# Performance work log

Hardware: AMD Instinct MI355X
Metric: run time of the kernel (lower is better)

The kernel has to match this reference:

```python
import jax, jax.numpy as jnp
import numpy as np

NUM_CLASSES = 22
CLIP_LENGTH = 256.0
OVERLAP_THRESH = 0.5
EPS = 1.1920929e-07  # torch.finfo(float32).eps
BOUNDS_LO = jnp.array([0., 15., 30., 60., 96., 256.], dtype=jnp.float32)
BOUNDS_HI = jnp.array([30., 60., 120., 240., 768., 768.], dtype=jnp.float32)


def setup_inputs() -> dict:
    key = jax.random.key(0)
    ks = jax.random.split(key, 9)
    B, K, C, N = 8, 100000, NUM_CLASSES, 32
    loc_data = jax.random.uniform(ks[0], (B, K, 2), jnp.float32)
    conf_data = jax.random.normal(ks[1], (B, K, C), jnp.float32)
    prop_loc_data = jax.random.uniform(ks[2], (B, K, 2), jnp.float32)
    prop_conf_data = jax.random.normal(ks[3], (B, K, C), jnp.float32)
    center_data = jax.random.normal(ks[4], (B, K, 1), jnp.float32)
    # priors: [K,2] = (center in [0,1], pyramid-level index 0..5)
    centers = (jnp.arange(K, dtype=jnp.float32) + 0.5) / K
    levels = jax.random.randint(ks[5], (K,), 0, 6).astype(jnp.float32)
    priors = jnp.stack([centers, levels], axis=-1)
    # targets: [B,N,3] = (start, end, label), label in 1..C-1
    starts = jax.random.uniform(ks[6], (B, N), jnp.float32, 0.0, 0.8)
    lens = jax.random.uniform(ks[7], (B, N), jnp.float32, 0.02, 0.3)
    ends = jnp.clip(starts + lens, 0.0, 1.0)
    labels = jax.random.randint(ks[8], (B, N), 1, C).astype(jnp.float32)
    targets = jnp.stack([starts, ends, labels], axis=-1)
    return {"loc_data": loc_data, "conf_data": conf_data,
            "prop_loc_data": prop_loc_data, "prop_conf_data": prop_conf_data,
            "center_data": center_data, "priors": priors, "targets": targets}


def _calc_iou(pred, tgt):
    # pred/tgt: [..., 2] = (left, right) distances; 1-D segment IoU
    inter = jnp.minimum(pred[..., 0], tgt[..., 0]) + jnp.minimum(pred[..., 1], tgt[..., 1])
    union = pred[..., 0] + pred[..., 1] + tgt[..., 0] + tgt[..., 1] - inter
    return inter / jnp.maximum(union, EPS)


def _giou_elem(pred, tgt):
    inter = jnp.minimum(pred[..., 0], tgt[..., 0]) + jnp.minimum(pred[..., 1], tgt[..., 1])
    union = pred[..., 0] + pred[..., 1] + tgt[..., 0] + tgt[..., 1] - inter
    ious = inter / jnp.maximum(union, EPS)
    ac = jnp.maximum(pred[..., 0], tgt[..., 0]) + jnp.maximum(pred[..., 1], tgt[..., 1])
    gious = ious - (ac - union) / jnp.maximum(ac, EPS)
    return 1.0 - gious


def _focal_sum(logits, tgt):
    # FocalLoss_Ori: softmax probs, pt = p[target]+1e-10, alpha[0]=0.25, alpha[1:]=0.75,
    # loss = -alpha_t * (1-pt)^2 * log(pt), summed over anchors -> [B]
    probs = jax.nn.softmax(logits, axis=-1)
    pt = jnp.take_along_axis(probs, tgt[..., None], axis=-1)[..., 0] + 1e-10
    alpha_t = jnp.where(tgt == 0, 0.25, 0.75)
    return (-alpha_t * (1.0 - pt) ** 2 * jnp.log(pt)).sum(axis=1)


def _forward(loc_data, conf_data, prop_loc_data, prop_conf_data, center_data, priors, targets):
    B, K, C = conf_data.shape
    maxn = 2.0 * CLIP_LENGTH

    def match():  # torch.no_grad() block
        center = priors[:, 0]                              # [K]
        lvl = priors[:, 1].astype(jnp.int32)
        lb = BOUNDS_LO[lvl][None, :, None]                 # [1,K,1]
        rb = BOUNDS_HI[lvl][None, :, None]
        ts, te = targets[..., 0], targets[..., 1]          # [B,N]
        left = (center[None, :, None] - ts[:, None, :]) * CLIP_LENGTH   # [B,K,N]
        right = (te[:, None, :] - center[None, :, None]) * CLIP_LENGTH
        max_dis = jnp.maximum(left, right)
        area = left + right
        bad = (left < 0) | (right < 0) | (max_dis <= lb) | (max_dis > rb)
        area = jnp.where(bad, maxn, area)
        best_area = area.min(axis=2)                       # [B,K]
        best_idx = area.argmin(axis=2)                     # [B,K]
        gs = jnp.take_along_axis(ts, best_idx, axis=1)
        ge = jnp.take_along_axis(te, best_idx, axis=1)
        loc_t = jnp.stack([(center[None, :] - gs) * CLIP_LENGTH,
                           (ge - center[None, :]) * CLIP_LENGTH], axis=-1)  # [B,K,2]
        labels = targets[..., 2]
        conf = jnp.take_along_axis(labels, best_idx, axis=1).astype(jnp.int32)
        conf = jnp.where(best_area >= maxn, 0, conf)
        iou = _calc_iou(loc_data, loc_t)                   # [B,K]
        pos = conf > 0
        has_pos = pos.any(axis=1)
        max_iou = jnp.where(has_pos, jnp.where(pos, iou, -jnp.inf).max(axis=1), 2.0)
        thr = jnp.minimum(OVERLAP_THRESH, max_iou)[:, None]
        prop_conf = jnp.where(iou < thr, 0, conf)
        prop_w = loc_data[..., 0] + loc_data[..., 1]
        prop_loc_t = (loc_t - loc_data) / (0.5 * prop_w[..., None])
        return loc_t, conf, prop_conf, prop_loc_t

    loc_t, conf_t, prop_conf_t, prop_loc_t = jax.lax.stop_gradient(match())
    pos = conf_t > 0                                       # [B,K]
    prop_pos = prop_conf_t > 0
    Nb = jnp.maximum(pos.sum(axis=1), 1).astype(jnp.float32)
    PNb = jnp.maximum(prop_pos.sum(axis=1), 1).astype(jnp.float32)

    # loc giou loss over positives
    loss_l = jnp.where(pos, _giou_elem(loc_data, loc_t), 0.0).sum(axis=1) / Nb

    # prop smooth_l1 over prop positives (beta=1)
    d = jnp.abs(prop_loc_data - prop_loc_t)
    sl1 = jnp.where(d < 1.0, 0.5 * d * d, d - 0.5).sum(axis=-1)   # [B,K]
    loss_prop_l = jnp.where(prop_pos, sl1, 0.0).sum(axis=1) / PNb

    # centerness BCE-with-logits vs refined IoU over positives
    prop_w = loc_data[..., 0] + loc_data[..., 1]
    cur_loc_p = 0.5 * prop_w[..., None] * prop_loc_data + loc_data
    ious_c = jnp.maximum(_calc_iou(cur_loc_p, loc_t), 0.0)
    x = center_data[..., 0]
    bce = jax.nn.softplus(x) - x * ious_c                  # BCEWithLogits(x, y)
    loss_ct = jnp.where(pos, bce, 0.0).sum(axis=1) / Nb

    # focal classification losses over ALL anchors
    loss_c = _focal_sum(conf_data, conf_t) / Nb
    loss_prop_c = _focal_sum(prop_conf_data, prop_conf_t) / PNb

    return jnp.stack([loss_l.mean(), loss_c.mean(), loss_prop_l.mean(),
                      loss_prop_c.mean(), loss_ct.mean()])


def reference(loc_data, conf_data, prop_loc_data, prop_conf_data, center_data, priors, targets):
    return _forward(loc_data, conf_data, prop_loc_data, prop_conf_data,
                    center_data, priors, targets)
```

## Files before the change

kernel.cpp:

```cpp
#include <hip/hip_runtime.h>
#include <math.h>

#define BLK 256
#define NCLS 22
#define EPSF 1.1920929e-07f
#define K1PR 4
#define K1CHUNK (BLK * K1PR)

__device__ __constant__ float c_lo[6] = {0.f, 15.f, 30.f, 60.f, 96.f, 256.f};
__device__ __constant__ float c_hi[6] = {30.f, 60.f, 120.f, 240.f, 768.f, 768.f};

struct MatchRes { float t0, t1; int conf; };

template <int NN>
__device__ inline MatchRes do_match_u(float center, int lvl, const float* tg) {
    float lb = c_lo[lvl], rb = c_hi[lvl];
    float best = 1e30f; int bidx = 0;
#pragma unroll
    for (int j = 0; j < NN; ++j) {
        float ts = tg[3 * j], te = tg[3 * j + 1];
        float left  = (center - ts) * 256.f;
        float right = (te - center) * 256.f;
        float md   = fmaxf(left, right);
        float area = left + right;
        bool bad = (left < 0.f) | (right < 0.f) | (md <= lb) | (md > rb);
        area = bad ? 512.f : area;
        if (area < best) { best = area; bidx = j; }
    }
    MatchRes r;
    float gs = tg[3 * bidx], ge = tg[3 * bidx + 1];
    r.t0 = (center - gs) * 256.f;
    r.t1 = (ge - center) * 256.f;
    r.conf = (best >= 512.f) ? 0 : (int)tg[3 * bidx + 2];
    return r;
}

__device__ inline MatchRes do_match_d(float center, int lvl, const float* tg, int N) {
    float lb = c_lo[lvl], rb = c_hi[lvl];
    float best = 1e30f; int bidx = 0;
    for (int j = 0; j < N; ++j) {
        float ts = tg[3 * j], te = tg[3 * j + 1];
        float left  = (center - ts) * 256.f;
        float right = (te - center) * 256.f;
        float md   = fmaxf(left, right);
        float area = left + right;
        bool bad = (left < 0.f) | (right < 0.f) | (md <= lb) | (md > rb);
        area = bad ? 512.f : area;
        if (area < best) { best = area; bidx = j; }
    }
    MatchRes r;
    float gs = tg[3 * bidx], ge = tg[3 * bidx + 1];
    r.t0 = (center - gs) * 256.f;
    r.t1 = (ge - center) * 256.f;
    r.conf = (best >= 512.f) ? 0 : (int)tg[3 * bidx + 2];
    return r;
}

__device__ inline float focal22v(const float2* q, int tgt) {
    float v[NCLS];
#pragma unroll
    for (int i = 0; i < NCLS / 2; ++i) { v[2 * i] = q[i].x; v[2 * i + 1] = q[i].y; }
    float m = v[0], xt = v[0];
#pragma unroll
    for (int i = 1; i < NCLS; ++i) {
        m = fmaxf(m, v[i]);
        xt = (i == tgt) ? v[i] : xt;
    }
    float s = 0.f;
#pragma unroll
    for (int i = 0; i < NCLS; ++i) s += __expf(v[i] - m);
    float pt = __expf(xt - m) / s + 1e-10f;
    float a = (tgt == 0) ? 0.25f : 0.75f;
    float om = 1.f - pt;
    return -a * om * om * __logf(pt);
}

__global__ __launch_bounds__(BLK) void k1_maxiou(const float* __restrict__ loc,
                                                 const float* __restrict__ priors,
                                                 const float* __restrict__ targets,
                                                 float* __restrict__ wsmax,
                                                 int K, int N) {
    int b = blockIdx.y;
    int chunk0 = blockIdx.x * K1CHUNK;
    __shared__ float tg[96];
    __shared__ float red[4];
    if (threadIdx.x < 3 * N) tg[threadIdx.x] = targets[b * 3 * N + threadIdx.x];
    __syncthreads();
    float my = -INFINITY;
    for (int it = 0; it < K1PR; ++it) {
        int k = chunk0 + it * BLK + threadIdx.x;
        if (k < K) {
            float2 pr = *reinterpret_cast<const float2*>(priors + 2 * k);
            MatchRes mr = (N == 32) ? do_match_u<32>(pr.x, (int)pr.y, tg)
                                    : do_match_d(pr.x, (int)pr.y, tg, N);
            if (mr.conf > 0) {
                size_t idx = (size_t)b * K + k;
                float2 p = *reinterpret_cast<const float2*>(loc + idx * 2);
                float inter = fminf(p.x, mr.t0) + fminf(p.y, mr.t1);
                float uni = p.x + p.y + mr.t0 + mr.t1 - inter;
                my = fmaxf(my, inter / fmaxf(uni, EPSF));
            }
        }
    }
#pragma unroll
    for (int off = 32; off; off >>= 1) my = fmaxf(my, __shfl_xor(my, off));
    int wid = threadIdx.x >> 6;
    if ((threadIdx.x & 63) == 0) red[wid] = my;
    __syncthreads();
    if (threadIdx.x == 0)
        wsmax[b * gridDim.x + blockIdx.x] =
            fmaxf(fmaxf(red[0], red[1]), fmaxf(red[2], red[3]));
}

__global__ __launch_bounds__(BLK, 4) void k2_loss(const float* __restrict__ loc,
                                                  const float* __restrict__ conf,
                                                  const float* __restrict__ ploc,
                                                  const float* __restrict__ pconf,
                                                  const float* __restrict__ cent,
                                                  const float* __restrict__ priors,
                                                  const float* __restrict__ targets,
                                                  const float* __restrict__ wsmax,
                                                  float* __restrict__ wspart,
                                                  int K, int N, int nb1) {
    int b = blockIdx.y;
    int k = blockIdx.x * BLK + threadIdx.x;
    int wid = threadIdx.x >> 6, lane = threadIdx.x & 63;
    __shared__ float tg[96];
    __shared__ float red[7][4];
    if (threadIdx.x < 3 * N) tg[threadIdx.x] = targets[b * 3 * N + threadIdx.x];
    __syncthreads();

    float mx = -INFINITY;
    for (int j = lane; j < nb1; j += 64) mx = fmaxf(mx, wsmax[b * nb1 + j]);
#pragma unroll
    for (int off = 32; off; off >>= 1) mx = fmaxf(mx, __shfl_xor(mx, off));
    float thr = (mx == -INFINITY) ? 0.5f : fminf(0.5f, mx);

    bool act = k < K;
    int kc = act ? k : K - 1;
    size_t idx = (size_t)b * K + kc;

    float2 cv[NCLS / 2], pv[NCLS / 2];
    {
        const float2* gc = reinterpret_cast<const float2*>(conf + idx * NCLS);
        const float2* gp = reinterpret_cast<const float2*>(pconf + idx * NCLS);
#pragma unroll
        for (int i = 0; i < NCLS / 2; ++i) cv[i] = gc[i];
#pragma unroll
        for (int i = 0; i < NCLS / 2; ++i) pv[i] = gp[i];
    }
    float2 p  = reinterpret_cast<const float2*>(loc)[idx];
    float2 pl = reinterpret_cast<const float2*>(ploc)[idx];
    float  xc = cent[idx];
    float2 pr = reinterpret_cast<const float2*>(priors)[kc];

    MatchRes mr = (N == 32) ? do_match_u<32>(pr.x, (int)pr.y, tg)
                            : do_match_d(pr.x, (int)pr.y, tg, N);

    float s_giou = 0.f, s_sl1 = 0.f, s_bce = 0.f, c_pos = 0.f, c_ppos = 0.f;
    float t0 = mr.t0, t1 = mr.t1;
    float inter = fminf(p.x, t0) + fminf(p.y, t1);
    float uni = p.x + p.y + t0 + t1 - inter;
    float iou = inter / fmaxf(uni, EPSF);
    bool pos = act && (mr.conf > 0);
    int pc = (iou < thr) ? 0 : mr.conf;
    float pw = p.x + p.y;
    if (pos) {
        c_pos = 1.f;
        float ac = fmaxf(p.x, t0) + fmaxf(p.y, t1);
        float g = iou - (ac - uni) / fmaxf(ac, EPSF);
        s_giou = 1.f - g;
        float cl0 = 0.5f * pw * pl.x + p.x;
        float cl1 = 0.5f * pw * pl.y + p.y;
        float i2 = fminf(cl0, t0) + fminf(cl1, t1);
        float u2 = cl0 + cl1 + t0 + t1 - i2;
        float iouc = fmaxf(i2 / fmaxf(u2, EPSF), 0.f);
        float sp = fmaxf(xc, 0.f) + log1pf(__expf(-fabsf(xc)));
        s_bce = sp - xc * iouc;
    }
    if (act && pc > 0) {
        c_ppos = 1.f;
        float hpw = 0.5f * pw;
        float plt0 = (t0 - p.x) / hpw;
        float plt1 = (t1 - p.y) / hpw;
        float d0 = fabsf(pl.x - plt0), d1 = fabsf(pl.y - plt1);
        float f0 = (d0 < 1.f) ? 0.5f * d0 * d0 : d0 - 0.5f;
        float f1 = (d1 < 1.f) ? 0.5f * d1 * d1 : d1 - 0.5f;
        s_sl1 = f0 + f1;
    }
    float s_fc  = act ? focal22v(cv, mr.conf) : 0.f;
    float s_fpc = act ? focal22v(pv, pc)      : 0.f;

#pragma unroll
    for (int off = 32; off; off >>= 1) {
        s_giou += __shfl_xor(s_giou, off);
        s_sl1  += __shfl_xor(s_sl1, off);
        s_bce  += __shfl_xor(s_bce, off);
        s_fc   += __shfl_xor(s_fc, off);
        s_fpc  += __shfl_xor(s_fpc, off);
        c_pos  += __shfl_xor(c_pos, off);
        c_ppos += __shfl_xor(c_ppos, off);
    }
    if ((threadIdx.x & 63) == 0) {
        red[0][wid] = s_giou; red[1][wid] = s_sl1; red[2][wid] = s_bce;
        red[3][wid] = s_fc;   red[4][wid] = s_fpc; red[5][wid] = c_pos;
        red[6][wid] = c_ppos;
    }
    __syncthreads();
    if (threadIdx.x < 7) {
        float v = red[threadIdx.x][0] + red[threadIdx.x][1] +
                  red[threadIdx.x][2] + red[threadIdx.x][3];
        wspart[((size_t)b * gridDim.x + blockIdx.x) * 8 + threadIdx.x] = v;
    }
}

__global__ __launch_bounds__(512) void k3_final(const float* __restrict__ wspart,
                                                float* __restrict__ out, int B, int nb2) {
    int w = threadIdx.x >> 6, lane = threadIdx.x & 63;
    __shared__ float ls[8][5];
    float s[7] = {0.f, 0.f, 0.f, 0.f, 0.f, 0.f, 0.f};
    if (w < B) {
        for (int e = lane; e < nb2; e += 64) {
            const float* a = wspart + ((size_t)w * nb2 + e) * 8;
#pragma unroll
            for (int i = 0; i < 7; ++i) s[i] += a[i];
        }
    }
#pragma unroll
    for (int off = 32; off; off >>= 1)
#pragma unroll
        for (int i = 0; i < 7; ++i) s[i] += __shfl_xor(s[i], off);
    if (w < B && lane == 0) {
        float Nb  = fmaxf(s[5], 1.f);
        float PNb = fmaxf(s[6], 1.f);
        ls[w][0] = s[0] / Nb;
        ls[w][1] = s[3] / Nb;
        ls[w][2] = s[1] / PNb;
        ls[w][3] = s[4] / PNb;
        ls[w][4] = s[2] / Nb;
    }
    __syncthreads();
    if (threadIdx.x < 5) {
        float t = 0.f;
        for (int bb = 0; bb < B; ++bb) t += ls[bb][threadIdx.x];
        out[threadIdx.x] = t / (float)B;
    }
}

extern "C" void kernel_launch(void* const* d_in, const int* in_sizes, int n_in,
                              void* d_out, int out_size, void* d_ws, size_t ws_size,
                              hipStream_t stream) {
    const float* loc     = (const float*)d_in[0];
    const float* conf    = (const float*)d_in[1];
    const float* ploc    = (const float*)d_in[2];
    const float* pconf   = (const float*)d_in[3];
    const float* cent    = (const float*)d_in[4];
    const float* priors  = (const float*)d_in[5];
    const float* targets = (const float*)d_in[6];
    int K = in_sizes[5] / 2;
    int B = in_sizes[0] / (2 * K);
    int N = in_sizes[6] / (3 * B);

    float* wsmax  = (float*)d_ws;
    float* wspart = (float*)d_ws + 1024;
    float* out = (float*)d_out;

    int nb1 = (K + K1CHUNK - 1) / K1CHUNK;
    int nb2 = (K + BLK - 1) / BLK;
    k1_maxiou<<<dim3(nb1, B), dim3(BLK), 0, stream>>>(loc, priors, targets, wsmax, K, N);
    k2_loss<<<dim3(nb2, B), dim3(BLK), 0, stream>>>(loc, conf, ploc, pconf, cent, priors,
                                                    targets, wsmax, wspart, K, N, nb1);
    k3_final<<<dim3(1), dim3(512), 0, stream>>>(wspart, out, B, nb2);
}
```

Measured before the change: 58.82 us.

## Cache match results from first pass and process two anchors per thread

The first kernel now matches two anchors per thread using float4 loads and, when the workspace is large enough, stores each anchor's matched target offsets, label and IoU to a buffer. The loss kernel reads that buffer instead of redoing the 32-target matching. It also handles two anchors per thread with float4 loads of the class logits and a focal loss that uses split max and sum chains. This removes the duplicated matching compute, at the cost of writing and reading about 16 bytes per anchor and using more registers per thread. It also drops the occupancy hint from the launch bounds.

```diff
diff --git a/kernel.cpp b/kernel.cpp
--- a/kernel.cpp
+++ b/kernel.cpp
@@ -4,8 +4,8 @@
 #define BLK 256
 #define NCLS 22
 #define EPSF 1.1920929e-07f
-#define K1PR 4
-#define K1CHUNK (BLK * K1PR)
+#define K1PAIRS 2
+#define K1CHUNK (BLK * 2 * K1PAIRS)
 
 __device__ __constant__ float c_lo[6] = {0.f, 15.f, 30.f, 60.f, 96.f, 256.f};
 __device__ __constant__ float c_hi[6] = {30.f, 60.f, 120.f, 240.f, 768.f, 768.f};
@@ -56,30 +56,53 @@
     return r;
 }
 
-__device__ inline float focal22v(const float2* q, int tgt) {
+__device__ inline float calc_iou(float px, float py, float t0, float t1) {
+    float inter = fminf(px, t0) + fminf(py, t1);
+    float uni = px + py + t0 + t1 - inter;
+    return inter / fmaxf(uni, EPSF);
+}
+
+__device__ inline float vget(const float4* a, int i) {
+    float4 x = a[i >> 2];
+    int r = i & 3;
+    return r == 0 ? x.x : (r == 1 ? x.y : (r == 2 ? x.z : x.w));
+}
+
+__device__ inline float focal22x(const float4* a, int base, int tgt) {
     float v[NCLS];
 #pragma unroll
-    for (int i = 0; i < NCLS / 2; ++i) { v[2 * i] = q[i].x; v[2 * i + 1] = q[i].y; }
-    float m = v[0], xt = v[0];
-#pragma unroll
-    for (int i = 1; i < NCLS; ++i) {
-        m = fmaxf(m, v[i]);
-        xt = (i == tgt) ? v[i] : xt;
-    }
-    float s = 0.f;
-#pragma unroll
-    for (int i = 0; i < NCLS; ++i) s += __expf(v[i] - m);
-    float pt = __expf(xt - m) / s + 1e-10f;
-    float a = (tgt == 0) ? 0.25f : 0.75f;
+    for (int i = 0; i < NCLS; ++i) v[i] = vget(a, base + i);
+    float m0 = v[0], m1 = v[1], m2 = v[2], m3 = v[3];
+#pragma unroll
+    for (int i = 4; i < NCLS; i += 4) {
+        m0 = fmaxf(m0, v[i]);
+        m1 = fmaxf(m1, v[i + 1]);
+        if (i + 2 < NCLS) m2 = fmaxf(m2, v[i + 2]);
+        if (i + 3 < NCLS) m3 = fmaxf(m3, v[i + 3]);
+    }
+    float m = fmaxf(fmaxf(m0, m1), fmaxf(m2, m3));
+    float sA = 0.f, sB = 0.f, eA = 0.f, eB = 0.f;
+#pragma unroll
+    for (int i = 0; i < NCLS; i += 2) {
+        float ea = __expf(v[i] - m);
+        float eb = __expf(v[i + 1] - m);
+        sA += ea; sB += eb;
+        eA += (i == tgt) ? ea : 0.f;
+        eB += (i + 1 == tgt) ? eb : 0.f;
+    }
+    float s = sA + sB;
+    float pt = (eA + eB) / s + 1e-10f;
+    float aa = (tgt == 0) ? 0.25f : 0.75f;
     float om = 1.f - pt;
-    return -a * om * om * __logf(pt);
-}
-
-__global__ __launch_bounds__(BLK) void k1_maxiou(const float* __restrict__ loc,
-                                                 const float* __restrict__ priors,
-                                                 const float* __restrict__ targets,
-                                                 float* __restrict__ wsmax,
-                                                 int K, int N) {
+    return -aa * om * om * __logf(pt);
+}
+
+__global__ __launch_bounds__(BLK) void k1_match(const float* __restrict__ loc,
+                                                const float* __restrict__ priors,
+                                                const float* __restrict__ targets,
+                                                float* __restrict__ wsmax,
+                                                float4* __restrict__ wsmatch,
+                                                int K, int N) {
     int b = blockIdx.y;
     int chunk0 = blockIdx.x * K1CHUNK;
     __shared__ float tg[96];
@@ -87,18 +110,24 @@
     if (threadIdx.x < 3 * N) tg[threadIdx.x] = targets[b * 3 * N + threadIdx.x];
     __syncthreads();
     float my = -INFINITY;
-    for (int it = 0; it < K1PR; ++it) {
-        int k = chunk0 + it * BLK + threadIdx.x;
-        if (k < K) {
-            float2 pr = *reinterpret_cast<const float2*>(priors + 2 * k);
-            MatchRes mr = (N == 32) ? do_match_u<32>(pr.x, (int)pr.y, tg)
+    for (int it = 0; it < K1PAIRS; ++it) {
+        int k0 = chunk0 + it * (BLK * 2) + threadIdx.x * 2;
+        if (k0 < K) {
+            size_t idx = (size_t)b * K + k0;
+            float4 pr = reinterpret_cast<const float4*>(priors)[k0 >> 1];
+            float4 lp = reinterpret_cast<const float4*>(loc)[idx >> 1];
+            MatchRes r0 = (N == 32) ? do_match_u<32>(pr.x, (int)pr.y, tg)
                                     : do_match_d(pr.x, (int)pr.y, tg, N);
-            if (mr.conf > 0) {
-                size_t idx = (size_t)b * K + k;
-                float2 p = *reinterpret_cast<const float2*>(loc + idx * 2);
-                float inter = fminf(p.x, mr.t0) + fminf(p.y, mr.t1);
-                float uni = p.x + p.y + mr.t0 + mr.t1 - inter;
-                my = fmaxf(my, inter / fmaxf(uni, EPSF));
+            MatchRes r1 = (N == 32) ? do_match_u<32>(pr.z, (int)pr.w, tg)
+                                    : do_match_d(pr.z, (int)pr.w, tg, N);
+            float i0 = calc_iou(lp.x, lp.y, r0.t0, r0.t1);
+            float i1 = calc_iou(lp.z, lp.w, r1.t0, r1.t1);
+            bool ok1 = (k0 + 1) < K;
+            if (r0.conf > 0) my = fmaxf(my, i0);
+            if (ok1 && r1.conf > 0) my = fmaxf(my, i1);
+            if (wsmatch) {
+                wsmatch[idx] = make_float4(r0.t0, r0.t1, (float)r0.conf, i0);
+                if (ok1) wsmatch[idx + 1] = make_float4(r1.t0, r1.t1, (float)r1.conf, i1);
             }
         }
     }
@@ -112,84 +141,114 @@
             fmaxf(fmaxf(red[0], red[1]), fmaxf(red[2], red[3]));
 }
 
-__global__ __launch_bounds__(BLK, 4) void k2_loss(const float* __restrict__ loc,
-                                                  const float* __restrict__ conf,
-                                                  const float* __restrict__ ploc,
-                                                  const float* __restrict__ pconf,
-                                                  const float* __restrict__ cent,
-                                                  const float* __restrict__ priors,
-                                                  const float* __restrict__ targets,
-                                                  const float* __restrict__ wsmax,
-                                                  float* __restrict__ wspart,
-                                                  int K, int N, int nb1) {
-    int b = blockIdx.y;
-    int k = blockIdx.x * BLK + threadIdx.x;
-    int wid = threadIdx.x >> 6, lane = threadIdx.x & 63;
-    __shared__ float tg[96];
-    __shared__ float red[7][4];
-    if (threadIdx.x < 3 * N) tg[threadIdx.x] = targets[b * 3 * N + threadIdx.x];
-    __syncthreads();
-
-    float mx = -INFINITY;
-    for (int j = lane; j < nb1; j += 64) mx = fmaxf(mx, wsmax[b * nb1 + j]);
-#pragma unroll
-    for (int off = 32; off; off >>= 1) mx = fmaxf(mx, __shfl_xor(mx, off));
-    float thr = (mx == -INFINITY) ? 0.5f : fminf(0.5f, mx);
-
-    bool act = k < K;
-    int kc = act ? k : K - 1;
-    size_t idx = (size_t)b * K + kc;
-
-    float2 cv[NCLS / 2], pv[NCLS / 2];
-    {
-        const float2* gc = reinterpret_cast<const float2*>(conf + idx * NCLS);
-        const float2* gp = reinterpret_cast<const float2*>(pconf + idx * NCLS);
-#pragma unroll
-        for (int i = 0; i < NCLS / 2; ++i) cv[i] = gc[i];
-#pragma unroll
-        for (int i = 0; i < NCLS / 2; ++i) pv[i] = gp[i];
-    }
-    float2 p  = reinterpret_cast<const float2*>(loc)[idx];
-    float2 pl = reinterpret_cast<const float2*>(ploc)[idx];
-    float  xc = cent[idx];
-    float2 pr = reinterpret_cast<const float2*>(priors)[kc];
-
-    MatchRes mr = (N == 32) ? do_match_u<32>(pr.x, (int)pr.y, tg)
-                            : do_match_d(pr.x, (int)pr.y, tg, N);
-
-    float s_giou = 0.f, s_sl1 = 0.f, s_bce = 0.f, c_pos = 0.f, c_ppos = 0.f;
-    float t0 = mr.t0, t1 = mr.t1;
-    float inter = fminf(p.x, t0) + fminf(p.y, t1);
-    float uni = p.x + p.y + t0 + t1 - inter;
-    float iou = inter / fmaxf(uni, EPSF);
-    bool pos = act && (mr.conf > 0);
-    int pc = (iou < thr) ? 0 : mr.conf;
-    float pw = p.x + p.y;
-    if (pos) {
-        c_pos = 1.f;
-        float ac = fmaxf(p.x, t0) + fmaxf(p.y, t1);
+__device__ inline void row_loss(bool act, float thr, float px, float py,
+                                float plx, float ply, float xc, float4 m,
+                                const float4* cr, int cbase,
+                                const float4* qr, int qbase,
+                                float& s_giou, float& s_sl1, float& s_bce,
+                                float& s_fc, float& s_fpc,
+                                float& c_pos, float& c_ppos) {
+    float t0 = m.x, t1 = m.y; int cf = (int)m.z; float iou = m.w;
+    int pc = (iou < thr) ? 0 : cf;
+    float pw = px + py;
+    if (act && cf > 0) {
+        c_pos += 1.f;
+        float inter = fminf(px, t0) + fminf(py, t1);
+        float uni = px + py + t0 + t1 - inter;
+        float ac = fmaxf(px, t0) + fmaxf(py, t1);
         float g = iou - (ac - uni) / fmaxf(ac, EPSF);
-        s_giou = 1.f - g;
-        float cl0 = 0.5f * pw * pl.x + p.x;
-        float cl1 = 0.5f * pw * pl.y + p.y;
+        s_giou += 1.f - g;
+        float cl0 = 0.5f * pw * plx + px;
+        float cl1 = 0.5f * pw * ply + py;
         float i2 = fminf(cl0, t0) + fminf(cl1, t1);
         float u2 = cl0 + cl1 + t0 + t1 - i2;
         float iouc = fmaxf(i2 / fmaxf(u2, EPSF), 0.f);
         float sp = fmaxf(xc, 0.f) + log1pf(__expf(-fabsf(xc)));
-        s_bce = sp - xc * iouc;
+        s_bce += sp - xc * iouc;
     }
     if (act && pc > 0) {
-        c_ppos = 1.f;
+        c_ppos += 1.f;
         float hpw = 0.5f * pw;
-        float plt0 = (t0 - p.x) / hpw;
-        float plt1 = (t1 - p.y) / hpw;
-        float d0 = fabsf(pl.x - plt0), d1 = fabsf(pl.y - plt1);
+        float plt0 = (t0 - px) / hpw;
+        float plt1 = (t1 - py) / hpw;
+        float d0 = fabsf(plx - plt0), d1 = fabsf(ply - plt1);
         float f0 = (d0 < 1.f) ? 0.5f * d0 * d0 : d0 - 0.5f;
         float f1 = (d1 < 1.f) ? 0.5f * d1 * d1 : d1 - 0.5f;
-        s_sl1 = f0 + f1;
-    }
-    float s_fc  = act ? focal22v(cv, mr.conf) : 0.f;
-    float s_fpc = act ? focal22v(pv, pc)      : 0.f;
+        s_sl1 += f0 + f1;
+    }
+    if (act) {
+        s_fc  += focal22x(cr, cbase, cf);
+        s_fpc += focal22x(qr, qbase, pc);
+    }
+}
+
+template <bool PREM>
+__global__ __launch_bounds__(BLK) void k2_loss(const float* __restrict__ loc,
+                                               const float* __restrict__ conf,
+                                               const float* __restrict__ ploc,
+                                               const float* __restrict__ pconf,
+                                               const float* __restrict__ cent,
+                                               const float* __restrict__ priors,
+                                               const float* __restrict__ targets,
+                                               const float* __restrict__ wsmax,
+                                               const float4* __restrict__ wsmatch,
+                                               float* __restrict__ wspart,
+                                               int K, int N, int nb1) {
+    int b = blockIdx.y;
+    int t = blockIdx.x * BLK + threadIdx.x;
+    int k0 = t * 2;
+    int wid = threadIdx.x >> 6, lane = threadIdx.x & 63;
+    __shared__ float tg[96];
+    __shared__ float red[7][4];
+    if (!PREM) {
+        if (threadIdx.x < 3 * N) tg[threadIdx.x] = targets[b * 3 * N + threadIdx.x];
+        __syncthreads();
+    }
+
+    float mx = -INFINITY;
+    for (int j = lane; j < nb1; j += 64) mx = fmaxf(mx, wsmax[b * nb1 + j]);
+#pragma unroll
+    for (int off = 32; off; off >>= 1) mx = fmaxf(mx, __shfl_xor(mx, off));
+    float thr = (mx == -INFINITY) ? 0.5f : fminf(0.5f, mx);
+
+    bool a0 = k0 < K;
+    int kc = a0 ? k0 : (K - 2);
+    bool a1 = a0 && ((k0 + 1) < K);
+    size_t idx = (size_t)b * K + kc;
+
+    float4 c4[11], q4[11];
+    {
+        const float4* gc = reinterpret_cast<const float4*>(conf + idx * NCLS);
+        const float4* gq = reinterpret_cast<const float4*>(pconf + idx * NCLS);
+#pragma unroll
+        for (int i = 0; i < 11; ++i) c4[i] = gc[i];
+#pragma unroll
+        for (int i = 0; i < 11; ++i) q4[i] = gq[i];
+    }
+    float4 lp = reinterpret_cast<const float4*>(loc)[idx >> 1];
+    float4 pp = reinterpret_cast<const float4*>(ploc)[idx >> 1];
+    float2 cc = reinterpret_cast<const float2*>(cent)[idx >> 1];
+
+    float4 m0, m1;
+    if (PREM) {
+        m0 = wsmatch[idx];
+        m1 = wsmatch[idx + 1];
+    } else {
+        float4 pr = reinterpret_cast<const float4*>(priors)[kc >> 1];
+        MatchRes r0 = (N == 32) ? do_match_u<32>(pr.x, (int)pr.y, tg)
+                                : do_match_d(pr.x, (int)pr.y, tg, N);
+        MatchRes r1 = (N == 32) ? do_match_u<32>(pr.z, (int)pr.w, tg)
+                                : do_match_d(pr.z, (int)pr.w, tg, N);
+        m0 = make_float4(r0.t0, r0.t1, (float)r0.conf, calc_iou(lp.x, lp.y, r0.t0, r0.t1));
+        m1 = make_float4(r1.t0, r1.t1, (float)r1.conf, calc_iou(lp.z, lp.w, r1.t0, r1.t1));
+    }
+
+    float s_giou = 0.f, s_sl1 = 0.f, s_bce = 0.f, s_fc = 0.f, s_fpc = 0.f,
+          c_pos = 0.f, c_ppos = 0.f;
+    row_loss(a0, thr, lp.x, lp.y, pp.x, pp.y, cc.x, m0, c4, 0, q4, 0,
+             s_giou, s_sl1, s_bce, s_fc, s_fpc, c_pos, c_ppos);
+    row_loss(a1, thr, lp.z, lp.w, pp.z, pp.w, cc.y, m1, c4, NCLS, q4, NCLS,
+             s_giou, s_sl1, s_bce, s_fc, s_fpc, c_pos, c_ppos);
 
 #pragma unroll
     for (int off = 32; off; off >>= 1) {
@@ -241,9 +300,9 @@
     }
     __syncthreads();
     if (threadIdx.x < 5) {
-        float t = 0.f;
-        for (int bb = 0; bb < B; ++bb) t += ls[bb][threadIdx.x];
-        out[threadIdx.x] = t / (float)B;
+        float tt = 0.f;
+        for (int bb = 0; bb < B; ++bb) tt += ls[bb][threadIdx.x];
+        out[threadIdx.x] = tt / (float)B;
     }
 }
 
@@ -263,12 +322,25 @@
 
     float* wsmax  = (float*)d_ws;
     float* wspart = (float*)d_ws + 1024;
+    const size_t match_off = (size_t)1 << 20;
+    float4* wsmatch = (float4*)((char*)d_ws + match_off);
     float* out = (float*)d_out;
 
     int nb1 = (K + K1CHUNK - 1) / K1CHUNK;
-    int nb2 = (K + BLK - 1) / BLK;
-    k1_maxiou<<<dim3(nb1, B), dim3(BLK), 0, stream>>>(loc, priors, targets, wsmax, K, N);
-    k2_loss<<<dim3(nb2, B), dim3(BLK), 0, stream>>>(loc, conf, ploc, pconf, cent, priors,
-                                                    targets, wsmax, wspart, K, N, nb1);
+    int rows_per_blk = BLK * 2;
+    int nb2 = (K + rows_per_blk - 1) / rows_per_blk;
+
+    bool prem = (ws_size >= match_off + (size_t)B * K * 16) &&
+                ((size_t)(1024 + B * nb2 * 8) * 4 <= match_off) &&
+                (K % 2 == 0);
+
+    k1_match<<<dim3(nb1, B), dim3(BLK), 0, stream>>>(loc, priors, targets, wsmax,
+                                                     prem ? wsmatch : nullptr, K, N);
+    if (prem)
+        k2_loss<true><<<dim3(nb2, B), dim3(BLK), 0, stream>>>(
+            loc, conf, ploc, pconf, cent, priors, targets, wsmax, wsmatch, wspart, K, N, nb1);
+    else
+        k2_loss<false><<<dim3(nb2, B), dim3(BLK), 0, stream>>>(
+            loc, conf, ploc, pconf, cent, priors, targets, wsmax, wsmatch, wspart, K, N, nb1);
     k3_final<<<dim3(1), dim3(512), 0, stream>>>(wspart, out, B, nb2);
 }
```

Result: faster. 55.34 us (-5.9%).
